# Optimization experiments

Measured on AMD Instinct MI355X. Metric: run time of the kernel, lower is better.

## Reference

```python
import jax, jax.numpy as jnp
import numpy as np

OUT = 7          # output_size
SR = 2           # sampling_ratio
SCALE = 1.0 / 16.0  # 1 / feature_stride


def _context_boxes(boxes):
    """8 surrounding cells of a 3x3 grid around each RoI; offset-major concat ([8N,4])."""
    x1, y1, x2, y2 = boxes[:, 0], boxes[:, 1], boxes[:, 2], boxes[:, 3]
    w = (x2 - x1) / 3.0
    h = (y2 - y1) / 3.0
    offs = []
    for i in range(3):
        for j in range(3):
            if i == 1 and j == 1:
                continue
            dx = j * w
            dy = i * h
            offs.append(jnp.stack([x1 + dx, y1 + dy, x1 + dx + w, y1 + dy + h], axis=1))
    return jnp.concatenate(offs, axis=0)


def _roi_align_v2(feat, boxes, scale, out, sr):
    """ROIAlignV2 (aligned=True). feat [C,H,W], boxes [B,4] xyxy -> [B,C,out,out]."""
    C, H, W = feat.shape
    # aligned: half-pixel offset, no max(roi_size, 1)
    x1 = boxes[:, 0] * scale - 0.5
    y1 = boxes[:, 1] * scale - 0.5
    bw = (boxes[:, 2] * scale - 0.5 - x1) / out   # bin width
    bh = (boxes[:, 3] * scale - 0.5 - y1) / out   # bin height
    # sample positions along each axis: start + (bin + (s+0.5)/sr) * bin_size  -> [B, out*sr]
    g = jnp.arange(out * sr) // sr
    s = jnp.arange(out * sr) % sr
    t = g + (s + 0.5) / sr                         # [out*sr]
    ys = y1[:, None] + t[None, :] * bh[:, None]    # [B,S]
    xs = x1[:, None] + t[None, :] * bw[:, None]    # [B,S]

    def axis(p, size):
        valid = (p >= -1.0) & (p <= size)
        p = jnp.clip(p, 0.0, size - 1.0)
        lo = jnp.clip(jnp.floor(p), 0.0, size - 2.0).astype(jnp.int32)
        return lo, p - lo, valid

    yl, fy, vy = axis(ys, H)
    xl, fx, vx = axis(xs, W)
    Y = yl[:, :, None]          # [B,S,1]
    X = xl[:, None, :]          # [B,1,S]
    f00 = feat[:, Y, X]         # [C,B,S,S]
    f01 = feat[:, Y, X + 1]
    f10 = feat[:, Y + 1, X]
    f11 = feat[:, Y + 1, X + 1]
    wy = fy[:, :, None]
    wx = fx[:, None, :]
    v = (f00 * (1 - wy) * (1 - wx) + f01 * (1 - wy) * wx
         + f10 * wy * (1 - wx) + f11 * wy * wx)
    v = v * (vy[:, :, None] & vx[:, None, :]).astype(v.dtype)
    # average the sr x sr samples inside each output bin
    B = boxes.shape[0]
    v = v.reshape(C, B, out, sr, out, sr).mean(axis=(3, 5))
    return v.transpose(1, 0, 2, 3)  # [B,C,out,out]


def setup_inputs() -> dict:
    key = jax.random.key(0)
    k1, k2, k3, k4 = jax.random.split(key, 4)
    features = jax.random.normal(k1, (256, 64, 64), dtype=jnp.float32)  # stride-16 map of a 1024px image
    N = 128
    xy = jax.random.uniform(k2, (N, 2), minval=0.0, maxval=800.0)
    wh = jax.random.uniform(k3, (N, 2), minval=32.0, maxval=220.0)
    boxes = jnp.concatenate([xy, xy + wh], axis=1)                      # [N,4] xyxy, image coords
    w_fuse = jax.random.normal(k4, (256, 2048), dtype=jnp.float32) * 0.02  # Conv2d(2048,256,1) weight
    b_fuse = jnp.zeros((256,), dtype=jnp.float32)
    return {"features": features, "boxes": boxes, "w_fuse": w_fuse, "b_fuse": b_fuse}


def reference(features, boxes, w_fuse, b_fuse):
    N = boxes.shape[0]
    cboxes = _context_boxes(boxes)                               # [8N,4] offset-major
    pooled = _roi_align_v2(features, cboxes, SCALE, OUT, SR)     # [8N,256,7,7]
    chunk = pooled.reshape(N, -1, OUT, OUT)                      # faithful to torch .view(N,-1,7,7)
    out = jnp.einsum('nchw,oc->nohw', chunk, w_fuse) + b_fuse[None, :, None, None]
    return jax.nn.relu(out)                                      # [N,256,7,7]
```

## Files before the change

### kernel.cpp

```cpp
#include <hip/hip_runtime.h>
#include <hip/hip_fp16.h>

#define SCALE (1.0f/16.0f)

typedef __attribute__((ext_vector_type(8))) _Float16 f16x8;
typedef __attribute__((ext_vector_type(4))) float f32x4;
typedef __attribute__((ext_vector_type(16))) float f32x16;
typedef __attribute__((ext_vector_type(4))) unsigned int u32x4;
typedef unsigned int u32;

#define PIN16(W) { _Pragma("unroll") \
    for (int s_ = 0; s_ < 16; ++s_) \
        asm volatile("" : "+v"((W)[s_][0]), "+v"((W)[s_][1]), "+v"((W)[s_][2]), "+v"((W)[s_][3])); }

__device__ __forceinline__ void gload16(const void* g, void* l) {
    __builtin_amdgcn_global_load_lds(
        (const __attribute__((address_space(1))) unsigned int*)g,
        (__attribute__((address_space(3))) unsigned int*)l, 16, 0, 0);
}
__device__ __forceinline__ __half2 asH2(u32 v) {
    union { u32 i; __half2 h; } u; u.i = v; return u.h;
}
__device__ __forceinline__ u32 asU32(__half2 h) {
    union { __half2 h; u32 i; } u; u.h = h; return u.i;
}
__device__ __forceinline__ int dupH2(float f) {
    __half h = __float2half_rn(f);
    __half2 d; d.x = h; d.y = h;
    union { __half2 h2; int i; } u; u.h2 = d; return u.i;
}

__global__ void k_prep(const float* __restrict__ feat, __half* __restrict__ featT,
                       const float* __restrict__ wf, __half* __restrict__ wr) {
    __shared__ float t[64][65];
    int b = blockIdx.x;
    if (b < 256) {
        int cb = (b >> 6) << 6;
        int pb = (b & 63) << 6;
        int lx = threadIdx.x & 63, ly = threadIdx.x >> 6;
#pragma unroll
        for (int i = 0; i < 16; ++i) {
            int cl = i*4 + ly;
            t[cl][lx] = feat[(size_t)(cb + cl) * 4096 + pb + lx];
        }
        __syncthreads();
#pragma unroll
        for (int i = 0; i < 16; ++i) {
            int pl = i*4 + ly;
            featT[(size_t)(pb + pl) * 256 + cb + lx] = __float2half_rn(t[lx][pl]);
        }
    } else {
        int ch = (b - 256) * 256 + threadIdx.x;
        int l  = ch & 63;
        int sk = (ch >> 6) & 15;
        int ot = (ch >> 10) & 7;
        int j  = ch >> 13;
        int o = ot*32 + (l & 31);
        int k = j*256 + sk*16 + (l >> 5)*8;
        const float* src = wf + (size_t)o*2048 + k;
        f32x4 a = *(const f32x4*)src;
        f32x4 bb = *(const f32x4*)(src + 4);
        f16x8 p;
#pragma unroll
        for (int u = 0; u < 4; ++u) p[u] = (_Float16)a[u];
#pragma unroll
        for (int u = 0; u < 4; ++u) p[4+u] = (_Float16)bb[u];
        *((f16x8*)wr + ch) = p;
    }
}

__global__ void __launch_bounds__(512) k_fused(
    const __half* __restrict__ featT,
    const float* __restrict__ boxes,
    const __half* __restrict__ wr,
    const float* __restrict__ bfuse,
    float* __restrict__ out)
{
    __shared__ char patch[2][28672];
    __shared__ char Pl[2][16384];
    __shared__ int4 tabs[4][2][7];
    __shared__ int  pbs[4][2];

    int tid = threadIdx.x;
    int lane = tid & 63, wid = tid >> 6;
    int r31 = lane & 31, l5 = lane >> 5;
    int bid = blockIdx.x;
    int n  = bid & 127;
    int hh = bid >> 7;
    int hw0 = hh * 32;
    int HWn = hh ? 17 : 32;
    bool producer = wid < 4;

    int nb_base = (n & 15) * 8;
    int off = n >> 4;
    int t3 = off + (off >= 4 ? 1 : 0);
    int ci = t3 / 3, cj = t3 - ci*3;

    {
        int padrows = 32 - HWn;
        for (int i = tid; i < padrows*32*2; i += 512) {
            int b = i / (padrows*32);
            int rem = i - b*(padrows*32);
            int row = HWn + (rem >> 5), slot = rem & 31;
            *(u32x4*)(Pl[b] + row*512 + slot*16) = (u32x4){0,0,0,0};
        }
    }

    auto tablesW = [&](int jj, int isy, bool active) {
        if (active) {
            int nbx = nb_base + jj;
            float bx1 = boxes[nbx*4+0], by1 = boxes[nbx*4+1];
            float bx2 = boxes[nbx*4+2], by2 = boxes[nbx*4+3];
            float w3 = (bx2-bx1)*(1.f/3.f), h3 = (by2-by1)*(1.f/3.f);
            float org  = isy ? (by1 + ci*h3)*SCALE - 0.5f : (bx1 + cj*w3)*SCALE - 0.5f;
            float step = (isy ? h3 : w3) * (SCALE*(1.f/14.f));
            float sc = isy ? 0.25f : 1.f;
            float p = org + ((float)lane + 0.5f)*step;
            float pc = fminf(fmaxf(p, 0.f), 63.f);
            float fl = fminf(floorf(pc), 62.f);
            float fr = pc - fl;
            float c0 = __shfl(fl, 2*lane);
            float c1 = __shfl(fl, 2*lane+1);
            float f  = __shfl(fr, 2*lane);
            float f2 = __shfl(fr, 2*lane+1);
            float fl0 = __shfl(fl, 0);
            int base = min((int)fl0, 56);
            float d = c1 - c0;
            float a0 = sc*((1.f-f) + (1.f-d)*(1.f-f2));
            float a1 = sc*(f + (1.f-d)*f2 + d*(1.f-f2));
            float a2 = sc*(d*f2);
            if (lane < 7) {
                int4 e;
                e.x = (int)c0 - base;
                e.y = dupH2(a0); e.z = dupH2(a1); e.w = dupH2(a2);
                tabs[jj & 3][isy][lane] = e;
            }
            if (lane == 0) pbs[jj & 3][isy] = base;
        }
    };

    auto stage = [&](int jj) {
        int xb = pbs[jj & 3][0], yb = pbs[jj & 3][1];
        char* pd = patch[jj & 1];
#pragma unroll
        for (int i = 0; i < 7; ++i) {
            int seg = wid + 4*i;
            int row = seg >> 2, q = seg & 3;
            const __half* src = featT + ((size_t)((yb + row)*64 + xb))*256 + q*512 + lane*8;
            gload16(src, pd + row*4096 + q*1024);
        }
    };

    auto pool = [&](int jj) {
        int buf = jj & 1;
        int co = tid & 31;
        int e0 = tid >> 5;
        const char* pb = patch[buf] + co*16;
        for (int e = e0; e < HWn; e += 8) {
            int g = hw0 + e;
            int h = (g*37) >> 8, w = g - h*7;
            int4 tx = tabs[jj & 3][0][w], ty = tabs[jj & 3][1][h];
            int px0 = tx.x, py0 = ty.x;
            int lx2 = min(px0 + 2, 7), ly2 = min(py0 + 2, 6);
            const char* r0 = pb + (py0*8 + px0)*512;
            const char* r1 = pb + (min(py0+1,6)*8 + px0)*512;
            const char* r2 = pb + (ly2*8 + px0)*512;
            int dx2 = (lx2 - px0)*512;
            u32x4 F00 = *(const u32x4*)(r0);
            u32x4 F01 = *(const u32x4*)(r0 + 512);
            u32x4 F02 = *(const u32x4*)(r0 + dx2);
            u32x4 F10 = *(const u32x4*)(r1);
            u32x4 F11 = *(const u32x4*)(r1 + 512);
            u32x4 F12 = *(const u32x4*)(r1 + dx2);
            u32x4 F20 = *(const u32x4*)(r2);
            u32x4 F21 = *(const u32x4*)(r2 + 512);
            u32x4 F22 = *(const u32x4*)(r2 + dx2);
            __half2 xa = asH2(tx.y), xb2 = asH2(tx.z), xc = asH2(tx.w);
            __half2 ya = asH2(ty.y), yb2 = asH2(ty.z), yc = asH2(ty.w);
            u32x4 res;
#pragma unroll
            for (int s = 0; s < 4; ++s) {
                __half2 q0 = __hfma2(asH2(F02[s]), xc, __hfma2(asH2(F01[s]), xb2, __hmul2(asH2(F00[s]), xa)));
                __half2 q1 = __hfma2(asH2(F12[s]), xc, __hfma2(asH2(F11[s]), xb2, __hmul2(asH2(F10[s]), xa)));
                __half2 q2 = __hfma2(asH2(F22[s]), xc, __hfma2(asH2(F21[s]), xb2, __hmul2(asH2(F20[s]), xa)));
                res[s] = asU32(__hfma2(q2, yc, __hfma2(q1, yb2, __hmul2(q0, ya))));
            }
            *(u32x4*)(Pl[buf] + e*512 + ((co*16) ^ ((e & 31) << 4))) = res;
        }
    };

    int cw = wid - 4;
    u32x4 Wf[32];
    f32x16 acc0, acc1;
#pragma unroll
    for (int i = 0; i < 16; ++i) { acc0[i] = 0.f; acc1[i] = 0.f; }

    auto prefW_half = [&](int j, int sb) {
#pragma unroll
        for (int t = 0; t < 2; ++t) {
            int otg = cw*2 + t;
            const u32x4* wb = (const u32x4*)wr + ((size_t)((j*8 + otg)*16))*64 + lane;
#pragma unroll
            for (int s = 0; s < 8; ++s) Wf[t*16 + sb*8 + s] = wb[(sb*8 + s)*64];
        }
    };

    auto gemm_half = [&](int j, int sb) {
        const char* plb = (j & 1) ? Pl[1] : Pl[0];
#pragma unroll
        for (int s = 0; s < 8; ++s) {
            int sk = sb*8 + s;
            int byo = r31*512 + ((sk*32 + l5*16) ^ (r31 << 4));
            f16x8 pf = *(const f16x8*)(plb + byo);
            acc0 = __builtin_amdgcn_mfma_f32_32x32x16_f16(
                __builtin_bit_cast(f16x8, Wf[sk]), pf, acc0, 0, 0, 0);
            acc1 = __builtin_amdgcn_mfma_f32_32x32x16_f16(
                __builtin_bit_cast(f16x8, Wf[16 + sk]), pf, acc1, 0, 0, 0);
        }
    };

    if (wid < 2) { tablesW(0, wid, true); tablesW(1, wid, true); tablesW(2, wid, true); }
    __syncthreads();
    if (producer) { stage(0); stage(1); }
    else          { prefW_half(0, 0); prefW_half(0, 1); PIN16(Wf); PIN16((Wf+16)); }
    __syncthreads();
    if (producer) pool(0);
    __syncthreads();

#pragma unroll
    for (int j = 0; j < 8; ++j) {
        if (producer) {
            if (j < 6) stage(j+2);
            if (j < 7) pool(j+1);
            if (j < 5) tablesW(j+3, wid, wid < 2);
        } else {
            gemm_half(j, 0);
            if (j < 7) prefW_half(j+1, 0);
            gemm_half(j, 1);
            if (j < 7) { prefW_half(j+1, 1); PIN16(Wf); PIN16((Wf+16)); }
        }
        __syncthreads();
    }

    if (!producer) {
        int hw = hw0 + r31;
        bool ok = r31 < HWn;
        float* ob = out + (size_t)n*12544 + hw;
#pragma unroll
        for (int t = 0; t < 2; ++t) {
            f32x16 a = t ? acc1 : acc0;
            int otb = (cw*2 + t)*32;
#pragma unroll
            for (int reg = 0; reg < 16; ++reg) {
                int o = otb + (reg & 3) + 8*(reg >> 2) + 4*l5;
                float v = a[reg] + bfuse[o];
                if (ok) ob[(size_t)o*49] = fmaxf(v, 0.f);
            }
        }
    }
}

extern "C" void kernel_launch(void* const* d_in, const int* in_sizes, int n_in,
                              void* d_out, int out_size, void* d_ws, size_t ws_size,
                              hipStream_t stream) {
    const float* feat  = (const float*)d_in[0];
    const float* boxes = (const float*)d_in[1];
    const float* wf    = (const float*)d_in[2];
    const float* bfuse = (const float*)d_in[3];
    float* out = (float*)d_out;

    char* ws = (char*)d_ws;
    __half* wr    = (__half*)ws;
    __half* featT = (__half*)(ws + (1u<<20));

    k_prep<<<512, 256, 0, stream>>>(feat, featT, wf, wr);
    k_fused<<<256, 512, 0, stream>>>(featT, boxes, wr, bfuse, out);
}
```

Before: 30.37 us.

## Triple-buffer feature patches with explicit vmcnt waits and raw barriers

Grows the patch staging buffer from two to three slots so async global-to-LDS loads can run two stages ahead of pooling. Full __syncthreads are replaced with partial vmcnt waits plus s_barrier, so loads stay in flight across iterations. Box coordinates are cached in LDS and the lookup tables are precomputed one stage further ahead. The register-pinning asm is removed. The cost is more LDS per block and hand-counted waitcnt values that are fragile if the compiler reorders or splits loads.

```diff
diff --git a/kernel.cpp b/kernel.cpp
--- a/kernel.cpp
+++ b/kernel.cpp
@@ -8,10 +8,6 @@
 typedef __attribute__((ext_vector_type(16))) float f32x16;
 typedef __attribute__((ext_vector_type(4))) unsigned int u32x4;
 typedef unsigned int u32;
-
-#define PIN16(W) { _Pragma("unroll") \
-    for (int s_ = 0; s_ < 16; ++s_) \
-        asm volatile("" : "+v"((W)[s_][0]), "+v"((W)[s_][1]), "+v"((W)[s_][2]), "+v"((W)[s_][3])); }
 
 __device__ __forceinline__ void gload16(const void* g, void* l) {
     __builtin_amdgcn_global_load_lds(
@@ -76,10 +72,11 @@
     const float* __restrict__ bfuse,
     float* __restrict__ out)
 {
-    __shared__ char patch[2][28672];
+    __shared__ char patch[3][28672];
     __shared__ char Pl[2][16384];
     __shared__ int4 tabs[4][2][7];
     __shared__ int  pbs[4][2];
+    __shared__ float bx_lds[32];
 
     int tid = threadIdx.x;
     int lane = tid & 63, wid = tid >> 6;
@@ -96,6 +93,7 @@
     int t3 = off + (off >= 4 ? 1 : 0);
     int ci = t3 / 3, cj = t3 - ci*3;
 
+    if (tid < 32) bx_lds[tid] = boxes[nb_base*4 + tid];
     {
         int padrows = 32 - HWn;
         for (int i = tid; i < padrows*32*2; i += 512) {
@@ -106,11 +104,11 @@
         }
     }
 
-    auto tablesW = [&](int jj, int isy, bool active) {
-        if (active) {
-            int nbx = nb_base + jj;
-            float bx1 = boxes[nbx*4+0], by1 = boxes[nbx*4+1];
-            float bx2 = boxes[nbx*4+2], by2 = boxes[nbx*4+3];
+    auto tablesW = [&](int jj) {
+        if (wid < 2) {
+            int isy = wid;
+            float bx1 = bx_lds[jj*4+0], by1 = bx_lds[jj*4+1];
+            float bx2 = bx_lds[jj*4+2], by2 = bx_lds[jj*4+3];
             float w3 = (bx2-bx1)*(1.f/3.f), h3 = (by2-by1)*(1.f/3.f);
             float org  = isy ? (by1 + ci*h3)*SCALE - 0.5f : (bx1 + cj*w3)*SCALE - 0.5f;
             float step = (isy ? h3 : w3) * (SCALE*(1.f/14.f));
@@ -141,7 +139,7 @@
 
     auto stage = [&](int jj) {
         int xb = pbs[jj & 3][0], yb = pbs[jj & 3][1];
-        char* pd = patch[jj & 1];
+        char* pd = patch[jj % 3];
 #pragma unroll
         for (int i = 0; i < 7; ++i) {
             int seg = wid + 4*i;
@@ -155,7 +153,7 @@
         int buf = jj & 1;
         int co = tid & 31;
         int e0 = tid >> 5;
-        const char* pb = patch[buf] + co*16;
+        const char* pb = patch[jj % 3] + co*16;
         for (int e = e0; e < HWn; e += 8) {
             int g = hw0 + e;
             int h = (g*37) >> 8, w = g - h*7;
@@ -219,27 +217,43 @@
         }
     };
 
-    if (wid < 2) { tablesW(0, wid, true); tablesW(1, wid, true); tablesW(2, wid, true); }
     __syncthreads();
-    if (producer) { stage(0); stage(1); }
-    else          { prefW_half(0, 0); prefW_half(0, 1); PIN16(Wf); PIN16((Wf+16)); }
+    tablesW(0); tablesW(1); tablesW(2); tablesW(3);
     __syncthreads();
-    if (producer) pool(0);
-    __syncthreads();
+    if (producer) {
+        stage(0); stage(1); stage(2);
+        asm volatile("s_waitcnt vmcnt(14)" ::: "memory");
+        __builtin_amdgcn_sched_barrier(0);
+        pool(0);
+        asm volatile("s_waitcnt lgkmcnt(0)" ::: "memory");
+    } else {
+        prefW_half(0, 0); prefW_half(0, 1);
+    }
+    __builtin_amdgcn_s_barrier();
+    __builtin_amdgcn_sched_barrier(0);
 
 #pragma unroll
     for (int j = 0; j < 8; ++j) {
         if (producer) {
-            if (j < 6) stage(j+2);
-            if (j < 7) pool(j+1);
-            if (j < 5) tablesW(j+3, wid, wid < 2);
+            if (j < 5) stage(j+3);
+            if (j < 7) {
+                if (j < 5)       asm volatile("s_waitcnt vmcnt(14)" ::: "memory");
+                else if (j == 5) asm volatile("s_waitcnt vmcnt(7)"  ::: "memory");
+                else             asm volatile("s_waitcnt vmcnt(0)"  ::: "memory");
+                __builtin_amdgcn_sched_barrier(0);
+                pool(j+1);
+            }
+            if (j < 4) tablesW(j+4);
+            asm volatile("s_waitcnt lgkmcnt(0)" ::: "memory");
         } else {
             gemm_half(j, 0);
             if (j < 7) prefW_half(j+1, 0);
             gemm_half(j, 1);
-            if (j < 7) { prefW_half(j+1, 1); PIN16(Wf); PIN16((Wf+16)); }
-        }
-        __syncthreads();
+            if (j < 7) prefW_half(j+1, 1);
+            asm volatile("s_waitcnt lgkmcnt(0)" ::: "memory");
+        }
+        __builtin_amdgcn_s_barrier();
+        __builtin_amdgcn_sched_barrier(0);
     }
 
     if (!producer) {
```

New measurement: 29.61 us. 2.5% less time.
